# Kernel optimization log

Hardware: AMD Instinct MI355X
Metric: run time of the kernel (lower is better)

## Reference

```python
import jax, jax.numpy as jnp
import numpy as np

SPARSITY_RATIO = 0.3


def setup_inputs() -> dict:
    key = jax.random.key(0)
    adj = jax.random.normal(key, (8, 2048, 2048), dtype=jnp.float32)
    return {"adj": adj}


def reference(adj):
    # k largest entries kept per row along the last axis (training-mode path)
    N = adj.shape[-1]
    k = max(1, int(N * (1.0 - SPARSITY_RATIO)))
    flat = adj.reshape(-1, N)                      # [B*N, N]
    _, topk_idx = jax.lax.top_k(flat, k)            # [B*N, k]
    rows = jnp.arange(flat.shape[0])[:, None]       # [B*N, 1]
    mask = jnp.zeros_like(flat).at[rows, topk_idx].set(1.0)
    return adj * mask.reshape(adj.shape)
```

## Files before the change

### kernel.cpp

```cpp
#include <hip/hip_runtime.h>


static constexpr int ROW_N   = 2048;
static constexpr int K_KEEP  = 1433;
static constexpr int THREADS = 256;
static constexpr int EPT     = 8;

struct Smem {
    alignas(16) unsigned hist[2048];
    unsigned wtot[4];
    unsigned bc_bin, bc_krem, bc_cnt;
};

__device__ __forceinline__ unsigned ord_f32(unsigned b) {
    unsigned m = (unsigned)((int)b >> 31);
    return b ^ (m | 0x80000000u);
}

template<int SHIFT, int NBITS, bool LAST>
__device__ __forceinline__ void radix_pass(Smem* sm, const unsigned (&u)[EPT],
                                           unsigned& alive, unsigned& krem,
                                           unsigned& tu, unsigned& cnt,
                                           int t, int lane, int w)
{
    constexpr int BINS = 1 << NBITS;
    constexpr int BPT  = BINS / THREADS;
    constexpr unsigned DMASK = (unsigned)(BINS - 1);

    uint4* hv = reinterpret_cast<uint4*>(&sm->hist[t * BPT]);
    #pragma unroll
    for (int i = 0; i < BPT / 4; ++i) hv[i] = make_uint4(0u, 0u, 0u, 0u);
    __syncthreads();

    if (alive) {
        #pragma unroll
        for (int i = 0; i < EPT; ++i) {
            if ((alive >> i) & 1u)
                atomicAdd(&sm->hist[(u[i] >> SHIFT) & DMASK], 1u);
        }
    }
    __syncthreads();

    unsigned h[BPT];
    #pragma unroll
    for (int i = 0; i < BPT / 4; ++i) {
        uint4 x = hv[i];
        h[4*i+0] = x.x; h[4*i+1] = x.y; h[4*i+2] = x.z; h[4*i+3] = x.w;
    }
    unsigned T = 0;
    #pragma unroll
    for (int i = 0; i < BPT; ++i) T += h[i];

    unsigned s = T;
    #pragma unroll
    for (int d = 1; d < 64; d <<= 1) {
        unsigned o = __shfl_down(s, d);
        s += (lane + d < 64) ? o : 0u;
    }
    if (lane == 0) sm->wtot[w] = s;
    __syncthreads();

    unsigned later = 0;
    #pragma unroll
    for (int w2 = 1; w2 < 4; ++w2)
        later += (w2 > w) ? sm->wtot[w2] : 0u;

    unsigned Snext = (s - T) + later;
    #pragma unroll
    for (int i = BPT - 1; i >= 0; --i) {
        unsigned S = Snext + h[i];
        if (S >= krem && Snext < krem) {
            sm->bc_bin  = (unsigned)(t * BPT + i);
            sm->bc_krem = krem - Snext;
            sm->bc_cnt  = h[i];
        }
        Snext = S;
    }
    __syncthreads();

    unsigned b = sm->bc_bin;
    krem = sm->bc_krem;
    cnt  = sm->bc_cnt;
    tu  |= (b << SHIFT);
    if (!LAST) {
        #pragma unroll
        for (int i = 0; i < EPT; ++i) {
            if (((u[i] >> SHIFT) & DMASK) != b) alive &= ~(1u << i);
        }
    }
}

__global__ __launch_bounds__(THREADS)
void topk_row_mask(const float* __restrict__ in, float* __restrict__ out) {
    __shared__ Smem sm;
    const int row  = blockIdx.x;
    const int t    = threadIdx.x;
    const int lane = t & 63;
    const int w    = t >> 6;

    const float4* rin  = reinterpret_cast<const float4*>(in)  + (size_t)row * (ROW_N / 4);
    float4*       rout = reinterpret_cast<float4*>(out)       + (size_t)row * (ROW_N / 4);

    const float4 va = rin[t * 2 + 0];
    const float4 vb = rin[t * 2 + 1];

    unsigned u[EPT];
    u[0] = ord_f32(__float_as_uint(va.x));
    u[1] = ord_f32(__float_as_uint(va.y));
    u[2] = ord_f32(__float_as_uint(va.z));
    u[3] = ord_f32(__float_as_uint(va.w));
    u[4] = ord_f32(__float_as_uint(vb.x));
    u[5] = ord_f32(__float_as_uint(vb.y));
    u[6] = ord_f32(__float_as_uint(vb.z));
    u[7] = ord_f32(__float_as_uint(vb.w));

    unsigned alive = 0xFFu;
    unsigned krem  = K_KEEP;
    unsigned tu    = 0;
    unsigned cnt   = 0;

    radix_pass<21, 11, false>(&sm, u, alive, krem, tu, cnt, t, lane, w);
    radix_pass<10, 11, false>(&sm, u, alive, krem, tu, cnt, t, lane, w);

    bool allkeep;
    if (cnt == 1u) {
        if (alive) {
            #pragma unroll
            for (int i = 0; i < EPT; ++i)
                if ((alive >> i) & 1u) sm.wtot[0] = u[i];
        }
        __syncthreads();
        tu   = sm.wtot[0];
        krem = 1u;
        allkeep = true;
    } else {
        radix_pass<0, 10, true>(&sm, u, alive, krem, tu, cnt, t, lane, w);
        allkeep = (krem == cnt);
    }

    if (allkeep) {
        float4 oa, ob;
        oa.x = (u[0] >= tu) ? va.x : 0.0f;
        oa.y = (u[1] >= tu) ? va.y : 0.0f;
        oa.z = (u[2] >= tu) ? va.z : 0.0f;
        oa.w = (u[3] >= tu) ? va.w : 0.0f;
        ob.x = (u[4] >= tu) ? vb.x : 0.0f;
        ob.y = (u[5] >= tu) ? vb.y : 0.0f;
        ob.z = (u[6] >= tu) ? vb.z : 0.0f;
        ob.w = (u[7] >= tu) ? vb.w : 0.0f;
        rout[t * 2 + 0] = oa;
        rout[t * 2 + 1] = ob;
    } else {
        unsigned ce = 0;
        #pragma unroll
        for (int i = 0; i < EPT; ++i) ce += (u[i] == tu) ? 1u : 0u;

        unsigned s2 = ce;
        #pragma unroll
        for (int d = 1; d < 64; d <<= 1) {
            unsigned o = __shfl_up(s2, d);
            s2 += (lane >= d) ? o : 0u;
        }
        if (lane == 63) sm.wtot[w] = s2;
        __syncthreads();
        unsigned basew = 0;
        #pragma unroll
        for (int w2 = 0; w2 < 3; ++w2)
            basew += (w2 < w) ? sm.wtot[w2] : 0u;
        unsigned rank = basew + s2 - ce;

        const float orig[EPT] = {va.x, va.y, va.z, va.w, vb.x, vb.y, vb.z, vb.w};
        float ov[EPT];
        #pragma unroll
        for (int i = 0; i < EPT; ++i) {
            bool keep;
            if (u[i] > tu) {
                keep = true;
            } else if (u[i] == tu) {
                keep = (rank < krem);
                rank++;
            } else {
                keep = false;
            }
            ov[i] = keep ? orig[i] : 0.0f;
        }
        rout[t * 2 + 0] = make_float4(ov[0], ov[1], ov[2], ov[3]);
        rout[t * 2 + 1] = make_float4(ov[4], ov[5], ov[6], ov[7]);
    }
}

extern "C" void kernel_launch(void* const* d_in, const int* in_sizes, int n_in,
                              void* d_out, int out_size, void* d_ws, size_t ws_size,
                              hipStream_t stream) {
    const float* in  = (const float*)d_in[0];
    float*       out = (float*)d_out;
    const int rows = in_sizes[0] / ROW_N;
    hipLaunchKernelGGL(topk_row_mask, dim3(rows), dim3(THREADS), 0, stream, in, out);
}
```

Before: 224.1 us.

## Replace three-pass radix select with one 12-bit histogram plus wave-level bitwise select

Replaces the three shared-memory radix histogram passes with a single 12-bit histogram over the top bits. The candidates that fall in the threshold bin are compacted into shared memory, and one wavefront then finds the exact k-th value by a bitwise ballot/popcount search. A fallback loops over chunks when the bin holds more than 64 entries. An XOR swizzle on histogram addresses is added to reduce LDS bank conflicts. This removes several block-wide barriers and atomic passes, at the cost of extra work serialised on a single wave.

Measured after the change: 226.0 us. Within noise of the previous version (+0.8%).

```diff
diff --git a/kernel.cpp b/kernel.cpp
--- a/kernel.cpp
+++ b/kernel.cpp
@@ -5,89 +5,23 @@
 static constexpr int K_KEEP  = 1433;
 static constexpr int THREADS = 256;
 static constexpr int EPT     = 8;
+static constexpr int NB0     = 12;
+static constexpr int BINS0   = 1 << NB0;
+static constexpr int BPT0    = BINS0 / THREADS;
+static constexpr int SH0     = 32 - NB0;
+static constexpr unsigned LOWMASK = (1u << SH0) - 1u;
 
 struct Smem {
-    alignas(16) unsigned hist[2048];
+    alignas(16) unsigned hist[BINS0];
     unsigned wtot[4];
     unsigned bc_bin, bc_krem, bc_cnt;
+    unsigned cctr;
+    unsigned r_tu, r_krem, r_cnteq;
 };
 
 __device__ __forceinline__ unsigned ord_f32(unsigned b) {
     unsigned m = (unsigned)((int)b >> 31);
     return b ^ (m | 0x80000000u);
-}
-
-template<int SHIFT, int NBITS, bool LAST>
-__device__ __forceinline__ void radix_pass(Smem* sm, const unsigned (&u)[EPT],
-                                           unsigned& alive, unsigned& krem,
-                                           unsigned& tu, unsigned& cnt,
-                                           int t, int lane, int w)
-{
-    constexpr int BINS = 1 << NBITS;
-    constexpr int BPT  = BINS / THREADS;
-    constexpr unsigned DMASK = (unsigned)(BINS - 1);
-
-    uint4* hv = reinterpret_cast<uint4*>(&sm->hist[t * BPT]);
-    #pragma unroll
-    for (int i = 0; i < BPT / 4; ++i) hv[i] = make_uint4(0u, 0u, 0u, 0u);
-    __syncthreads();
-
-    if (alive) {
-        #pragma unroll
-        for (int i = 0; i < EPT; ++i) {
-            if ((alive >> i) & 1u)
-                atomicAdd(&sm->hist[(u[i] >> SHIFT) & DMASK], 1u);
-        }
-    }
-    __syncthreads();
-
-    unsigned h[BPT];
-    #pragma unroll
-    for (int i = 0; i < BPT / 4; ++i) {
-        uint4 x = hv[i];
-        h[4*i+0] = x.x; h[4*i+1] = x.y; h[4*i+2] = x.z; h[4*i+3] = x.w;
-    }
-    unsigned T = 0;
-    #pragma unroll
-    for (int i = 0; i < BPT; ++i) T += h[i];
-
-    unsigned s = T;
-    #pragma unroll
-    for (int d = 1; d < 64; d <<= 1) {
-        unsigned o = __shfl_down(s, d);
-        s += (lane + d < 64) ? o : 0u;
-    }
-    if (lane == 0) sm->wtot[w] = s;
-    __syncthreads();
-
-    unsigned later = 0;
-    #pragma unroll
-    for (int w2 = 1; w2 < 4; ++w2)
-        later += (w2 > w) ? sm->wtot[w2] : 0u;
-
-    unsigned Snext = (s - T) + later;
-    #pragma unroll
-    for (int i = BPT - 1; i >= 0; --i) {
-        unsigned S = Snext + h[i];
-        if (S >= krem && Snext < krem) {
-            sm->bc_bin  = (unsigned)(t * BPT + i);
-            sm->bc_krem = krem - Snext;
-            sm->bc_cnt  = h[i];
-        }
-        Snext = S;
-    }
-    __syncthreads();
-
-    unsigned b = sm->bc_bin;
-    krem = sm->bc_krem;
-    cnt  = sm->bc_cnt;
-    tu  |= (b << SHIFT);
-    if (!LAST) {
-        #pragma unroll
-        for (int i = 0; i < EPT; ++i) {
-            if (((u[i] >> SHIFT) & DMASK) != b) alive &= ~(1u << i);
-        }
-    }
 }
 
 __global__ __launch_bounds__(THREADS)
@@ -97,6 +31,7 @@
     const int t    = threadIdx.x;
     const int lane = t & 63;
     const int w    = t >> 6;
+    const int xr   = (t >> 1) & 3;
 
     const float4* rin  = reinterpret_cast<const float4*>(in)  + (size_t)row * (ROW_N / 4);
     float4*       rout = reinterpret_cast<float4*>(out)       + (size_t)row * (ROW_N / 4);
@@ -114,31 +49,138 @@
     u[6] = ord_f32(__float_as_uint(vb.z));
     u[7] = ord_f32(__float_as_uint(vb.w));
 
-    unsigned alive = 0xFFu;
-    unsigned krem  = K_KEEP;
-    unsigned tu    = 0;
-    unsigned cnt   = 0;
-
-    radix_pass<21, 11, false>(&sm, u, alive, krem, tu, cnt, t, lane, w);
-    radix_pass<10, 11, false>(&sm, u, alive, krem, tu, cnt, t, lane, w);
-
-    bool allkeep;
-    if (cnt == 1u) {
-        if (alive) {
+    {
+        uint4* hq = reinterpret_cast<uint4*>(sm.hist);
+        const uint4 z = make_uint4(0u, 0u, 0u, 0u);
+        #pragma unroll
+        for (int i = 0; i < 4; ++i) hq[t * 4 + (i ^ xr)] = z;
+        if (t == 0) sm.cctr = 0u;
+    }
+    __syncthreads();
+
+    #pragma unroll
+    for (int i = 0; i < EPT; ++i) {
+        unsigned g = u[i] >> SH0;
+        atomicAdd(&sm.hist[g ^ ((g >> 3) & 0xCu)], 1u);
+    }
+    __syncthreads();
+
+    unsigned T = 0;
+    {
+        uint4* hq = reinterpret_cast<uint4*>(sm.hist);
+        #pragma unroll
+        for (int i = 0; i < 4; ++i) {
+            uint4 x = hq[t * 4 + (i ^ xr)];
+            T += x.x + x.y + x.z + x.w;
+        }
+    }
+
+    unsigned s = T;
+    #pragma unroll
+    for (int d = 1; d < 64; d <<= 1) {
+        unsigned o = __shfl_down(s, d);
+        s += (lane + d < 64) ? o : 0u;
+    }
+    if (lane == 0) sm.wtot[w] = s;
+    __syncthreads();
+
+    unsigned later = 0;
+    #pragma unroll
+    for (int w2 = 1; w2 < 4; ++w2) later += (w2 > w) ? sm.wtot[w2] : 0u;
+    const unsigned Sabove = (s - T) + later;
+
+    if (Sabove < K_KEEP && Sabove + T >= K_KEEP) {
+        unsigned Snext = Sabove;
+        for (int i = BPT0 - 1; i >= 0; --i) {
+            unsigned phys = (unsigned)(t * BPT0) + ((((unsigned)(i >> 2) ^ (unsigned)xr) << 2) | (unsigned)(i & 3));
+            unsigned hb = sm.hist[phys];
+            unsigned S = Snext + hb;
+            if (S >= K_KEEP && Snext < K_KEEP) {
+                sm.bc_bin  = (unsigned)(t * BPT0 + i);
+                sm.bc_krem = (unsigned)K_KEEP - Snext;
+                sm.bc_cnt  = hb;
+            }
+            Snext = S;
+        }
+    }
+    __syncthreads();
+
+    const unsigned b    = sm.bc_bin;
+    const unsigned krem = sm.bc_krem;
+    const unsigned cnt  = sm.bc_cnt;
+
+    #pragma unroll
+    for (int i = 0; i < EPT; ++i) {
+        if ((u[i] >> SH0) == b) {
+            unsigned p = atomicAdd(&sm.cctr, 1u);
+            sm.hist[p] = u[i] & LOWMASK;
+        }
+    }
+    __syncthreads();
+
+    if (w == 0) {
+        if (cnt <= 64u) {
+            unsigned v = (lane < (int)cnt) ? sm.hist[lane] : 0u;
+            bool act = (lane < (int)cnt);
+            unsigned kr = krem;
             #pragma unroll
-            for (int i = 0; i < EPT; ++i)
-                if ((alive >> i) & 1u) sm.wtot[0] = u[i];
-        }
-        __syncthreads();
-        tu   = sm.wtot[0];
-        krem = 1u;
-        allkeep = true;
-    } else {
-        radix_pass<0, 10, true>(&sm, u, alive, krem, tu, cnt, t, lane, w);
-        allkeep = (krem == cnt);
-    }
-
-    if (allkeep) {
+            for (int bpos = SH0 - 1; bpos >= 0; --bpos) {
+                bool bitset = ((v >> bpos) & 1u) != 0u;
+                bool pb = act && bitset;
+                unsigned c = (unsigned)__popcll(__ballot(pb));
+                if (c >= kr) {
+                    act = pb;
+                } else {
+                    kr -= c;
+                    act = act && !bitset;
+                }
+            }
+            unsigned long long eq = __ballot(act);
+            unsigned cnteq = (unsigned)__popcll(eq);
+            int fl = __ffsll(eq) - 1;
+            unsigned tl = __shfl(v, fl);
+            if (lane == 0) {
+                sm.r_tu    = (b << SH0) | tl;
+                sm.r_krem  = kr;
+                sm.r_cnteq = cnteq;
+            }
+        } else {
+            unsigned kr  = krem;
+            unsigned pfx = 0u;
+            const int nc = ((int)cnt + 63) >> 6;
+            for (int bpos = SH0 - 1; bpos >= 0; --bpos) {
+                unsigned c = 0;
+                for (int base = 0; base < nc; ++base) {
+                    int idx = base * 64 + lane;
+                    unsigned v = (idx < (int)cnt) ? sm.hist[idx] : 0u;
+                    bool p = (idx < (int)cnt) &&
+                             ((v >> (bpos + 1)) == (pfx >> (bpos + 1))) &&
+                             (((v >> bpos) & 1u) != 0u);
+                    c += (unsigned)__popcll(__ballot(p));
+                }
+                if (c >= kr) pfx |= (1u << bpos);
+                else         kr  -= c;
+            }
+            unsigned cnteq = 0;
+            for (int base = 0; base < nc; ++base) {
+                int idx = base * 64 + lane;
+                bool p = (idx < (int)cnt) && (sm.hist[idx] == pfx);
+                cnteq += (unsigned)__popcll(__ballot(p));
+            }
+            if (lane == 0) {
+                sm.r_tu    = (b << SH0) | pfx;
+                sm.r_krem  = kr;
+                sm.r_cnteq = cnteq;
+            }
+        }
+    }
+    __syncthreads();
+
+    const unsigned tu    = sm.r_tu;
+    const unsigned kq    = sm.r_krem;
+    const unsigned cnteq = sm.r_cnteq;
+
+    if (kq == cnteq) {
         float4 oa, ob;
         oa.x = (u[0] >= tu) ? va.x : 0.0f;
         oa.y = (u[1] >= tu) ? va.y : 0.0f;
@@ -165,8 +207,7 @@
         __syncthreads();
         unsigned basew = 0;
         #pragma unroll
-        for (int w2 = 0; w2 < 3; ++w2)
-            basew += (w2 < w) ? sm.wtot[w2] : 0u;
+        for (int w2 = 0; w2 < 3; ++w2) basew += (w2 < w) ? sm.wtot[w2] : 0u;
         unsigned rank = basew + s2 - ce;
 
         const float orig[EPT] = {va.x, va.y, va.z, va.w, vb.x, vb.y, vb.z, vb.w};
@@ -177,7 +218,7 @@
             if (u[i] > tu) {
                 keep = true;
             } else if (u[i] == tu) {
-                keep = (rank < krem);
+                keep = (rank < kq);
                 rank++;
             } else {
                 keep = false;
```
